# Kernel optimization log

Measured on AMD Instinct MI355X. Metric: run time of the kernel, lower is better.

## Reference

```python
import jax, jax.numpy as jnp
import numpy as np
import math

D = 768       # hidden_size
FF = 3072     # intermediate_size
H = 12        # num heads
L = 3         # decoder_num_hidden_layers
R = 4         # max_role_embeddings
CS = 512      # const_size
B = 256
C = 32
EPS = 1e-5


def _inorm(x):
    # InstanceNorm1d with affine=False on (N, C, L): normalize over last dim
    m = jnp.mean(x, axis=-1, keepdims=True)
    v = jnp.var(x, axis=-1, keepdims=True)
    return (x - m) * jax.lax.rsqrt(v + EPS)


def _mlp(x, w1, b1, w2, b2):
    h = jax.nn.gelu(x @ w1.T + b1, approximate=False)
    return h @ w2.T + b2


def _tree_layer(x, pe, iw, ib, ow, ob, w1, b1, w2, b2):
    # x: (N, 2, D); pe: (N, 2, D)
    qk_in = x + pe
    Wq, Wk, Wv = jnp.split(iw, 3, axis=0)
    bq, bk, bv = jnp.split(ib, 3)
    N = x.shape[0]
    hd = D // H
    q = (qk_in @ Wq.T + bq).reshape(N, 2, H, hd)
    k = (qk_in @ Wk.T + bk).reshape(N, 2, H, hd)
    v = (x @ Wv.T + bv).reshape(N, 2, H, hd)
    scores = jnp.einsum('nqhd,nkhd->nhqk', q, k) / math.sqrt(hd)
    a = jax.nn.softmax(scores, axis=-1)
    o = jnp.einsum('nhqk,nkhd->nqhd', a, v).reshape(N, 2, D)
    o = o @ ow.T + ob
    x = _inorm(x + o)
    f = jax.nn.gelu(x @ w1.T + b1, approximate=False) @ w2.T + b2
    x = _inorm(x + f)
    return x


def setup_inputs() -> dict:
    key = jax.random.key(0)
    ks = jax.random.split(key, 24)
    rn = lambda k, shape, s=0.02: jax.random.normal(k, shape, jnp.float32) * s
    inp = {
        'parent_ij': jax.random.normal(ks[0], (B, D), jnp.float32),
        'child_ikj': jax.random.normal(ks[1], (B, C, 2, D), jnp.float32),
        'parent_scores': jax.random.normal(ks[2], (B, 1), jnp.float32),
        'child_scores': jax.random.normal(ks[3], (B, C, 2), jnp.float32),
        'attn_in_w': rn(ks[4], (L, 3 * D, D)),
        'attn_in_b': rn(ks[5], (L, 3 * D)),
        'attn_out_w': rn(ks[6], (L, D, D)),
        'attn_out_b': rn(ks[7], (L, D)),
        'lin1_w': rn(ks[8], (L, FF, D)),
        'lin1_b': rn(ks[9], (L, FF)),
        'lin2_w': rn(ks[10], (L, D, FF)),
        'lin2_b': rn(ks[11], (L, D)),
        'pos_emb': rn(ks[12], (L, R, D)),
        'parent_w1': rn(ks[13], (D, D)), 'parent_b1': rn(ks[14], (D,)),
        'parent_w2': rn(ks[15], (CS, D)), 'parent_b2': rn(ks[16], (CS,)),
        'left_w1': rn(ks[17], (D, D)), 'left_b1': rn(ks[18], (D,)),
        'left_w2': rn(ks[19], (CS, D)), 'left_b2': rn(ks[20], (CS,)),
        'right_w1': rn(ks[21], (D, D)), 'right_b1': rn(ks[22], (D,)),
        'right_w2': rn(ks[23], (CS, D)), 'right_b2': rn(jax.random.fold_in(key, 99), (CS,)),
    }
    return inp


def reference(parent_ij, child_ikj, parent_scores, child_scores,
              attn_in_w, attn_in_b, attn_out_w, attn_out_b,
              lin1_w, lin1_b, lin2_w, lin2_b, pos_emb,
              parent_w1, parent_b1, parent_w2, parent_b2,
              left_w1, left_b1, left_w2, left_b2,
              right_w1, right_b1, right_w2, right_b2):
    b, c = child_ikj.shape[0], child_ikj.shape[1]
    N = b * c * 2
    # inputs: token0 = parent, token1 = flipped child; row parity 0 -> right child, 1 -> left child
    parent_ext = jnp.broadcast_to(parent_ij[:, None, None, :], (b, c, 2, D))
    child_flip = child_ikj[:, :, ::-1, :]
    x = jnp.stack([parent_ext, child_flip], axis=3).reshape(N, 2, D)

    # scoring heads (parent row is identical for even/odd rows)
    pc = _mlp(parent_ij, parent_w1, parent_b1, parent_w2, parent_b2)          # (b, CS)
    rc = _mlp(child_ikj[:, :, 1, :], right_w1, right_b1, right_w2, right_b2)  # (b, c, CS)
    lc = _mlp(child_ikj[:, :, 0, :], left_w1, left_b1, left_w2, left_b2)      # (b, c, CS)
    scale = 1.0 / math.sqrt(CS)
    left_score = jnp.einsum('bs,bcs->bc', pc, rc) * scale
    right_score = jnp.einsum('bs,bcs->bc', pc, lc) * scale
    outside_scores = jnp.stack([left_score, right_score], axis=2)  # (b, c, 2)

    role_ids = jnp.array([[0, 1], [0, 2]])  # (2, 2) roles for even/odd rows
    for l in range(L):
        pe = jnp.broadcast_to(pos_emb[l][role_ids][None], (b * c, 2, 2, D)).reshape(N, 2, D)
        x = _tree_layer(x, pe, attn_in_w[l], attn_in_b[l], attn_out_w[l], attn_out_b[l],
                        lin1_w[l], lin1_b[l], lin2_w[l], lin2_b[l])

    out_e_ij = _inorm(x.sum(axis=1)).reshape(b, c, 2, D)
    return outside_scores, out_e_ij
```

## Files before the change

kernel.cpp:

```cpp
#include <hip/hip_runtime.h>
#include <cstdint>
#include <cmath>

#define DD      768
#define FFD     3072
#define NH      12
#define HDIM    64
#define LAYERS  3
#define CSZ     512
#define NB      256
#define NC      32
#define NSEQ    (NB * NC * 2)
#define NTOK    (NSEQ * 2)

typedef unsigned short ushort_t;
using short8 = __attribute__((ext_vector_type(8))) short;
using f32x4  = __attribute__((ext_vector_type(4))) float;

static __device__ __forceinline__ float b2f(ushort_t u) {
    union { float f; uint32_t i; } x; x.i = ((uint32_t)u) << 16; return x.f;
}
static __device__ __forceinline__ ushort_t f2b(float f) {
    uint32_t i = __float_as_uint(f);
    uint32_t r = (i + 0x7fffu + ((i >> 16) & 1u)) >> 16;
    return (ushort_t)r;
}
static __device__ __forceinline__ float gelu_f(float x) {
    return 0.5f * x * (1.0f + erff(x * 0.70710678118654752f));
}
static __device__ __forceinline__ float wave_sum64(float v) {
#pragma unroll
    for (int off = 32; off > 0; off >>= 1) v += __shfl_xor(v, off, 64);
    return v;
}
static __device__ __forceinline__ void async_cp16(const void* g, void* l) {
    __builtin_amdgcn_global_load_lds((const __attribute__((address_space(1))) void*)g,
                                     (__attribute__((address_space(3))) void*)l, 16, 0, 0);
}
static __device__ __forceinline__ void wg_barrier() {
    asm volatile("" ::: "memory");
    __builtin_amdgcn_s_barrier();
    asm volatile("" ::: "memory");
}
#define WAITVM(N) asm volatile("s_waitcnt vmcnt(" #N ")" ::: "memory")
#define LDSFENCE() asm volatile("s_waitcnt lgkmcnt(0)" ::: "memory")

__global__ __launch_bounds__(256) void cvt_bf16(const float* __restrict__ s,
                                                ushort_t* __restrict__ d, int n) {
    const int i = (blockIdx.x * 256 + threadIdx.x) * 4;
    if (i < n) {
        const float4 v = *(const float4*)(s + i);
        ushort4 o;
        o.x = f2b(v.x); o.y = f2b(v.y); o.z = f2b(v.z); o.w = f2b(v.w);
        *(ushort4*)(d + i) = o;
    }
}

__global__ __launch_bounds__(192) void build_x(const float* __restrict__ parent,
                                               const float* __restrict__ child,
                                               ushort_t* __restrict__ X) {
    const int r = blockIdx.x;
    const int t = threadIdx.x;
    const int n = r >> 1, q = r & 1;
    const int i = n >> 6;
    const int k = (n >> 1) & 31;
    const int j = n & 1;
    const float* src = (q == 0) ? (parent + (size_t)i * DD)
                                : (child + ((size_t)((i * 32 + k) * 2 + (1 - j))) * DD);
    const float4 v = ((const float4*)src)[t];
    ushort4 o;
    o.x = f2b(v.x); o.y = f2b(v.y); o.z = f2b(v.z); o.w = f2b(v.w);
    ((ushort4*)(X + (size_t)r * DD))[t] = o;
}

__global__ __launch_bounds__(256) void gemm_bf16(const ushort_t* __restrict__ A, int lda,
                                                 const ushort_t* __restrict__ W,
                                                 const float* __restrict__ bias,
                                                 ushort_t* __restrict__ C, int ldc,
                                                 int K, int NT, int GM, int GN,
                                                 int dogelu) {
    __shared__ __align__(16) short smem[16384];
    short* As = smem;
    short* Bs = smem + 8192;

    const int st = blockIdx.x / (GM * GN);
    const int stn = NT / GN;
    const int srow = st / stn, scol = st - srow * stn;
    const int r = blockIdx.x - st * (GM * GN);
    const int mt = srow * GM + r / GN;
    const int nt = scol * GN + (r - (r / GN) * GN);
    const int m0 = mt * 128;
    const int n0 = nt * 128;

    const int tid = threadIdx.x;
    const int r0s = tid >> 2, c0s = (tid & 3) * 8;
    const ushort_t* Ag0 = A + (size_t)(m0 + r0s) * lda + c0s;
    const ushort_t* Ag1 = A + (size_t)(m0 + 64 + r0s) * lda + c0s;
    const ushort_t* Wg0 = W + (size_t)(n0 + r0s) * K + c0s;
    const ushort_t* Wg1 = W + (size_t)(n0 + 64 + r0s) * K + c0s;

    const int wid = tid >> 6, lane = tid & 63;
    const int wm = (wid >> 1) * 64, wn = (wid & 1) * 64;
    const int lm = lane & 15;
    const int ko = (lane >> 4) * 8;

    f32x4 acc[4][4];
#pragma unroll
    for (int i = 0; i < 4; ++i)
#pragma unroll
        for (int j = 0; j < 4; ++j) acc[i][j] = {0.f, 0.f, 0.f, 0.f};

    {
        async_cp16(Ag0, As + tid * 8);
        async_cp16(Ag1, As + 2048 + tid * 8);
        async_cp16(Wg0, Bs + tid * 8);
        async_cp16(Wg1, Bs + 2048 + tid * 8);
    }

    for (int k0 = 0; k0 < K; k0 += 32) {
        const int b = (k0 >> 5) & 1;
        const int boff = b * 4096;
        __syncthreads();
        if (k0 + 32 < K) {
            const int o = (boff ^ 4096);
            const int k = k0 + 32;
            async_cp16(Ag0 + k, As + o + tid * 8);
            async_cp16(Ag1 + k, As + o + 2048 + tid * 8);
            async_cp16(Wg0 + k, Bs + o + tid * 8);
            async_cp16(Wg1 + k, Bs + o + 2048 + tid * 8);
        }
        short8 af[4], bfr[4];
#pragma unroll
        for (int i = 0; i < 4; ++i)
            af[i] = *(const short8*)(As + boff + (wm + i * 16 + lm) * 32 + ko);
#pragma unroll
        for (int j = 0; j < 4; ++j)
            bfr[j] = *(const short8*)(Bs + boff + (wn + j * 16 + lm) * 32 + ko);
#pragma unroll
        for (int i = 0; i < 4; ++i)
#pragma unroll
            for (int j = 0; j < 4; ++j)
                acc[i][j] = __builtin_amdgcn_mfma_f32_16x16x32_bf16(af[i], bfr[j], acc[i][j], 0, 0, 0);
    }

    float* T = (float*)smem;
    float* Tw = T + wid * 1088;
    const int r4 = lane >> 4;
    const int rrow = lane >> 2;
    const int rc0 = (lane & 3) * 16;
    const int gcolb = n0 + wn;

    float4 bb[4];
    if (bias) {
#pragma unroll
        for (int t = 0; t < 4; ++t) bb[t] = *(const float4*)(bias + gcolb + rc0 + t * 4);
    } else {
#pragma unroll
        for (int t = 0; t < 4; ++t) bb[t] = make_float4(0.f, 0.f, 0.f, 0.f);
    }

#pragma unroll
    for (int i = 0; i < 4; ++i) {
        __syncthreads();
#pragma unroll
        for (int j = 0; j < 4; ++j)
#pragma unroll
            for (int rr = 0; rr < 4; ++rr)
                Tw[(r4 * 4 + rr) * 68 + j * 16 + lm] = acc[i][j][rr];
        __syncthreads();
        float o[16];
#pragma unroll
        for (int t = 0; t < 4; ++t)
            *(f32x4*)&o[t * 4] = *(const f32x4*)(Tw + rrow * 68 + rc0 + t * 4);
#pragma unroll
        for (int t = 0; t < 4; ++t) {
            o[t * 4 + 0] += ((const float*)&bb[t])[0];
            o[t * 4 + 1] += ((const float*)&bb[t])[1];
            o[t * 4 + 2] += ((const float*)&bb[t])[2];
            o[t * 4 + 3] += ((const float*)&bb[t])[3];
        }
        if (dogelu) {
#pragma unroll
            for (int t = 0; t < 16; ++t) o[t] = gelu_f(o[t]);
        }
        uint32_t pk[8];
#pragma unroll
        for (int t = 0; t < 8; ++t)
            pk[t] = (uint32_t)f2b(o[2 * t]) | ((uint32_t)f2b(o[2 * t + 1]) << 16);
        ushort_t* dst = C + (size_t)(m0 + wm + i * 16 + rrow) * ldc + gcolb + rc0;
        *(uint4*)dst = make_uint4(pk[0], pk[1], pk[2], pk[3]);
        *(uint4*)(dst + 8) = make_uint4(pk[4], pk[5], pk[6], pk[7]);
    }
}

__global__ __launch_bounds__(512, 2) void gemm256(const ushort_t* __restrict__ A, int lda,
                                                  const ushort_t* __restrict__ W,
                                                  const float* __restrict__ bias,
                                                  ushort_t* __restrict__ C, int ldc,
                                                  int K, int NT, int GM, int GN,
                                                  int dogelu) {
    __shared__ __align__(16) short smem[65536];
    const int tid = threadIdx.x;

    const int nwg = gridDim.x;
    const int bid = blockIdx.x;
    const int qx = nwg >> 3, rx = nwg & 7;
    const int xcd = bid & 7, pos = bid >> 3;
    const int wgid = (xcd < rx ? xcd * (qx + 1) : rx * (qx + 1) + (xcd - rx) * qx) + pos;
    const int stb = GM * GN;
    const int st = wgid / stb;
    const int stn = NT / GN;
    const int srow = st / stn, scol = st - srow * stn;
    const int r = wgid - st * stb;
    const int mt = srow * GM + r / GN;
    const int nt = scol * GN + (r - (r / GN) * GN);
    const int m0 = mt * 256, n0 = nt * 256;

    const int srow_t = tid >> 2;
    const int scol_t = ((tid & 3) ^ ((tid >> 3) & 3)) << 3;
    const ushort_t* Ag = A + (size_t)(m0 + srow_t) * lda + scol_t;
    const ushort_t* Bg = W + (size_t)(n0 + srow_t) * K + scol_t;
    short* ldsA = smem + tid * 8;
    short* ldsB = smem + 8192 + tid * 8;
    const size_t ldaH = (size_t)128 * lda;
    const size_t ldbH = (size_t)128 * K;

    auto stage2A = [&](int kt_) {
        const int b_ = (kt_ & 3) * 16384;
        const int k_ = kt_ * 32;
        async_cp16(Ag + k_,        ldsA + b_);
        async_cp16(Ag + ldaH + k_, ldsA + b_ + 4096);
    };
    auto stage2B = [&](int kt_) {
        const int b_ = (kt_ & 3) * 16384;
        const int k_ = kt_ * 32;
        async_cp16(Bg + k_,        ldsB + b_);
        async_cp16(Bg + ldbH + k_, ldsB + b_ + 4096);
    };

    const int wid = tid >> 6, lane = tid & 63;
    const int wr = wid >> 2, wc = wid & 3;
    const int lm = lane & 15;
    const int swz = (((lane >> 4) ^ ((lane >> 1) & 3)) << 3);
    const short* rdA = smem + (wr * 128 + lm) * 32 + swz;
    const short* rdB = smem + 8192 + (wc * 64 + lm) * 32 + swz;

    f32x4 acc[8][4];
#pragma unroll
    for (int i = 0; i < 8; ++i)
#pragma unroll
        for (int j = 0; j < 4; ++j) acc[i][j] = {0.f, 0.f, 0.f, 0.f};

    const int NKT = K >> 5;
    stage2A(0); stage2B(0); stage2A(1); stage2B(1); stage2A(2); stage2B(2);
    WAITVM(8);
    wg_barrier();

    for (int kt = 0; kt < NKT; ++kt) {
        const int boff = (kt & 3) * 16384;
        short8 af[4], bfr[4], ag[4];
#pragma unroll
        for (int j = 0; j < 4; ++j) bfr[j] = *(const short8*)(rdB + boff + j * 512);
#pragma unroll
        for (int i = 0; i < 4; ++i) af[i] = *(const short8*)(rdA + boff + i * 512);
        if (kt + 3 < NKT) stage2A(kt + 3);
        wg_barrier();
        LDSFENCE();
        __builtin_amdgcn_s_setprio(1);
#pragma unroll
        for (int i = 0; i < 4; ++i)
#pragma unroll
            for (int j = 0; j < 4; ++j)
                acc[i][j] = __builtin_amdgcn_mfma_f32_16x16x32_bf16(af[i], bfr[j], acc[i][j], 0, 0, 0);
        __builtin_amdgcn_s_setprio(0);
        wg_barrier();
#pragma unroll
        for (int i = 0; i < 4; ++i) ag[i] = *(const short8*)(rdA + boff + (4 + i) * 512);
        if (kt + 3 < NKT) stage2B(kt + 3);
        if (kt + 3 < NKT)      { WAITVM(8); }
        else if (kt + 2 < NKT) { WAITVM(4); }
        else                   { WAITVM(0); }
        wg_barrier();
        LDSFENCE();
        __builtin_amdgcn_s_setprio(1);
#pragma unroll
        for (int i = 0; i < 4; ++i)
#pragma unroll
            for (int j = 0; j < 4; ++j)
                acc[4 + i][j] = __builtin_amdgcn_mfma_f32_16x16x32_bf16(ag[i], bfr[j], acc[4 + i][j], 0, 0, 0);
        __builtin_amdgcn_s_setprio(0);
        wg_barrier();
    }

    float* T = (float*)smem;
    float* Tw = T + wid * 1088;
    const int r4 = lane >> 4;
    const int rrow = lane >> 2;
    const int rc0 = (lane & 3) * 16;
    const int gcolb = n0 + wc * 64;

    float4 bb[4];
#pragma unroll
    for (int t = 0; t < 4; ++t) bb[t] = *(const float4*)(bias + gcolb + rc0 + t * 4);

#pragma unroll
    for (int mi = 0; mi < 8; ++mi) {
#pragma unroll
        for (int j = 0; j < 4; ++j)
#pragma unroll
            for (int rr = 0; rr < 4; ++rr)
                Tw[(r4 * 4 + rr) * 68 + j * 16 + lm] = acc[mi][j][rr];
        LDSFENCE();
        float o[16];
#pragma unroll
        for (int t = 0; t < 4; ++t)
            *(f32x4*)&o[t * 4] = *(const f32x4*)(Tw + rrow * 68 + rc0 + t * 4);
#pragma unroll
        for (int t = 0; t < 4; ++t) {
            o[t * 4 + 0] += ((const float*)&bb[t])[0];
            o[t * 4 + 1] += ((const float*)&bb[t])[1];
            o[t * 4 + 2] += ((const float*)&bb[t])[2];
            o[t * 4 + 3] += ((const float*)&bb[t])[3];
        }
        if (dogelu) {
#pragma unroll
            for (int t = 0; t < 16; ++t) o[t] = gelu_f(o[t]);
        }
        uint32_t pk[8];
#pragma unroll
        for (int t = 0; t < 8; ++t)
            pk[t] = (uint32_t)f2b(o[2 * t]) | ((uint32_t)f2b(o[2 * t + 1]) << 16);
        ushort_t* dst = C + (size_t)(m0 + wr * 128 + mi * 16 + rrow) * ldc + gcolb + rc0;
        *(uint4*)dst = make_uint4(pk[0], pk[1], pk[2], pk[3]);
        *(uint4*)(dst + 8) = make_uint4(pk[4], pk[5], pk[6], pk[7]);
        LDSFENCE();
    }
}

__global__ __launch_bounds__(256) void pe_proj(const float* __restrict__ pel,
                                               const float* __restrict__ aiwl,
                                               float* __restrict__ PEQ,
                                               float* __restrict__ PEK) {
    const int wid = threadIdx.x >> 6, lane = threadIdx.x & 63;
    const int task = blockIdx.x * 4 + wid;
    const int which = task >= 3 * DD;
    const int idx = task - which * 3 * DD;
    const int r = idx / DD, o = idx - r * DD;
    const float* pe = pel + (size_t)r * DD;
    const float* w = aiwl + (size_t)(which ? DD + o : o) * DD;
    float s = 0.f;
#pragma unroll
    for (int e = 0; e < 12; ++e) s += pe[e * 64 + lane] * w[e * 64 + lane];
    s = wave_sum64(s);
    if (lane == 0) (which ? PEK : PEQ)[r * DD + o] = s;
}

__global__ __launch_bounds__(256) void attn_kernel(const ushort_t* __restrict__ QKV,
                                                   const float* __restrict__ peq,
                                                   const float* __restrict__ pek,
                                                   ushort_t* __restrict__ O,
                                                   int seq0) {
    const int wid = threadIdx.x >> 6;
    const int lane = threadIdx.x & 63;
    const int task = blockIdx.x * 4 + wid;
    const int ns = task / NH;
    const int h = task - ns * NH;
    const int j = (seq0 + ns) & 1;
    const ushort_t* base = QKV + (size_t)(2 * ns) * (3 * DD);
    const int c = h * HDIM + lane;
    const int role1 = (1 + j) * DD;

    const float q0 = b2f(base[c]) + peq[c];
    const float k0 = b2f(base[DD + c]) + pek[c];
    const float v0 = b2f(base[2 * DD + c]);
    const ushort_t* base1 = base + 3 * DD;
    const float q1 = b2f(base1[c]) + peq[role1 + c];
    const float k1 = b2f(base1[DD + c]) + pek[role1 + c];
    const float v1 = b2f(base1[2 * DD + c]);

    float p00 = q0 * k0, p01 = q0 * k1, p10 = q1 * k0, p11 = q1 * k1;
#pragma unroll
    for (int off = 32; off > 0; off >>= 1) {
        p00 += __shfl_xor(p00, off, 64);
        p01 += __shfl_xor(p01, off, 64);
        p10 += __shfl_xor(p10, off, 64);
        p11 += __shfl_xor(p11, off, 64);
    }
    const float sc = 0.125f;
    const float s00 = p00 * sc, s01 = p01 * sc, s10 = p10 * sc, s11 = p11 * sc;

    const float m0 = fmaxf(s00, s01);
    const float e00 = __expf(s00 - m0), e01 = __expf(s01 - m0);
    const float a00 = e00 / (e00 + e01);
    const float o0 = a00 * v0 + (1.0f - a00) * v1;

    const float m1 = fmaxf(s10, s11);
    const float e10 = __expf(s10 - m1), e11 = __expf(s11 - m1);
    const float a10 = e10 / (e10 + e11);
    const float o1 = a10 * v0 + (1.0f - a10) * v1;

    O[(size_t)(2 * ns) * DD + c] = f2b(o0);
    O[(size_t)(2 * ns + 1) * DD + c] = f2b(o1);
}

__global__ __launch_bounds__(256) void add_inorm(ushort_t* __restrict__ x,
                                                 const ushort_t* __restrict__ d) {
    const int wid = threadIdx.x >> 6, lane = threadIdx.x & 63;
    const int r = blockIdx.x * 4 + wid;
    ushort_t* xr = x + (size_t)r * DD;
    const ushort_t* dr = d + (size_t)r * DD;
    float v[12];
    float s = 0.f, ss = 0.f;
#pragma unroll
    for (int e = 0; e < 3; ++e) {
        const ushort4 xa = ((const ushort4*)xr)[e * 64 + lane];
        const ushort4 da = ((const ushort4*)dr)[e * 64 + lane];
        const float a0 = b2f(xa.x) + b2f(da.x);
        const float a1 = b2f(xa.y) + b2f(da.y);
        const float a2 = b2f(xa.z) + b2f(da.z);
        const float a3 = b2f(xa.w) + b2f(da.w);
        v[e * 4 + 0] = a0; v[e * 4 + 1] = a1; v[e * 4 + 2] = a2; v[e * 4 + 3] = a3;
        s += a0 + a1 + a2 + a3;
        ss += a0 * a0 + a1 * a1 + a2 * a2 + a3 * a3;
    }
    s = wave_sum64(s); ss = wave_sum64(ss);
    const float mean = s * (1.0f / DD);
    const float var = ss * (1.0f / DD) - mean * mean;
    const float rs = rsqrtf(var + 1e-5f);
#pragma unroll
    for (int e = 0; e < 3; ++e) {
        ushort4 o;
        o.x = f2b((v[e * 4 + 0] - mean) * rs);
        o.y = f2b((v[e * 4 + 1] - mean) * rs);
        o.z = f2b((v[e * 4 + 2] - mean) * rs);
        o.w = f2b((v[e * 4 + 3] - mean) * rs);
        ((ushort4*)xr)[e * 64 + lane] = o;
    }
}

__global__ __launch_bounds__(256) void final_inorm(const ushort_t* __restrict__ x,
                                                   float* __restrict__ out) {
    const int wid = threadIdx.x >> 6, lane = threadIdx.x & 63;
    const int n = blockIdx.x * 4 + wid;
    const ushort_t* r0 = x + (size_t)(2 * n) * DD;
    const ushort_t* r1 = r0 + DD;
    float v[12];
    float s = 0.f, ss = 0.f;
#pragma unroll
    for (int e = 0; e < 3; ++e) {
        const ushort4 xa = ((const ushort4*)r0)[e * 64 + lane];
        const ushort4 xb = ((const ushort4*)r1)[e * 64 + lane];
        const float a0 = b2f(xa.x) + b2f(xb.x);
        const float a1 = b2f(xa.y) + b2f(xb.y);
        const float a2 = b2f(xa.z) + b2f(xb.z);
        const float a3 = b2f(xa.w) + b2f(xb.w);
        v[e * 4 + 0] = a0; v[e * 4 + 1] = a1; v[e * 4 + 2] = a2; v[e * 4 + 3] = a3;
        s += a0 + a1 + a2 + a3;
        ss += a0 * a0 + a1 * a1 + a2 * a2 + a3 * a3;
    }
    s = wave_sum64(s); ss = wave_sum64(ss);
    const float mean = s * (1.0f / DD);
    const float var = ss * (1.0f / DD) - mean * mean;
    const float rs = rsqrtf(var + 1e-5f);
    float* orow = out + (size_t)n * DD;
#pragma unroll
    for (int e = 0; e < 3; ++e) {
        float4 o;
        o.x = (v[e * 4 + 0] - mean) * rs;
        o.y = (v[e * 4 + 1] - mean) * rs;
        o.z = (v[e * 4 + 2] - mean) * rs;
        o.w = (v[e * 4 + 3] - mean) * rs;
        ((float4*)orow)[e * 64 + lane] = o;
    }
}

__global__ __launch_bounds__(256) void score_dot(const ushort_t* __restrict__ pc,
                                                 const ushort_t* __restrict__ cc,
                                                 float* __restrict__ out, int which) {
    const int wid = threadIdx.x >> 6;
    const int lane = threadIdx.x & 63;
    const int row = blockIdx.x * 4 + wid;
    const int b = row >> 5;
    const ushort_t* p = pc + (size_t)b * CSZ;
    const ushort_t* c = cc + (size_t)row * CSZ;
    float s = 0.f;
#pragma unroll
    for (int e = 0; e < 8; ++e) s += b2f(p[e * 64 + lane]) * b2f(c[e * 64 + lane]);
    s = wave_sum64(s);
    if (lane == 0) out[row * 2 + which] = s * 0.04419417382415922f;
}

extern "C" void kernel_launch(void* const* d_in, const int* in_sizes, int n_in,
                              void* d_out, int out_size, void* d_ws, size_t ws_size,
                              hipStream_t stream) {
    const float* parent = (const float*)d_in[0];
    const float* child  = (const float*)d_in[1];
    const float* aiw = (const float*)d_in[4];
    const float* aib = (const float*)d_in[5];
    const float* aow = (const float*)d_in[6];
    const float* aob = (const float*)d_in[7];
    const float* l1w = (const float*)d_in[8];
    const float* l1b = (const float*)d_in[9];
    const float* l2w = (const float*)d_in[10];
    const float* l2b = (const float*)d_in[11];
    const float* pemb = (const float*)d_in[12];
    const float* pw1 = (const float*)d_in[13];
    const float* pb1 = (const float*)d_in[14];
    const float* pw2 = (const float*)d_in[15];
    const float* pb2 = (const float*)d_in[16];
    const float* lw1 = (const float*)d_in[17];
    const float* lb1 = (const float*)d_in[18];
    const float* lw2 = (const float*)d_in[19];
    const float* lb2 = (const float*)d_in[20];
    const float* rw1 = (const float*)d_in[21];
    const float* rb1 = (const float*)d_in[22];
    const float* rw2 = (const float*)d_in[23];
    const float* rb2 = (const float*)d_in[24];
    float* out = (float*)d_out;
    (void)in_sizes; (void)n_in; (void)out_size;

    int CH = 8192;
    {
        const size_t fixedB = 100ull * 1024 * 1024;
        if (ws_size >= fixedB + (size_t)32768 * 4608 * 2) CH = 32768;
        else if (ws_size >= fixedB + (size_t)16384 * 4608 * 2) CH = 16384;
    }
    const int NCH = NTOK / CH;

    ushort_t* W0 = (ushort_t*)d_ws;
    size_t off = 0;
    auto take = [&](size_t elems) { ushort_t* p = W0 + off; off += (elems + 127) & ~(size_t)127; return p; };
    ushort_t* aiw_b = take((size_t)LAYERS * 3 * DD * DD);
    ushort_t* aow_b = take((size_t)LAYERS * DD * DD);
    ushort_t* l1w_b = take((size_t)LAYERS * FFD * DD);
    ushort_t* l2w_b = take((size_t)LAYERS * DD * FFD);
    ushort_t* pw1_b = take((size_t)DD * DD);
    ushort_t* pw2_b = take((size_t)CSZ * DD);
    ushort_t* lw1_b = take((size_t)DD * DD);
    ushort_t* lw2_b = take((size_t)CSZ * DD);
    ushort_t* rw1_b = take((size_t)DD * DD);
    ushort_t* rw2_b = take((size_t)CSZ * DD);
    ushort_t* Pb    = take((size_t)NB * DD);
    ushort_t* Xb    = take((size_t)NTOK * DD);
    ushort_t* S1b   = take((size_t)CH * FFD);
    ushort_t* S2b   = take((size_t)CH * DD);
    ushort_t* S3b   = take((size_t)CH * DD);
    ushort_t* P1b   = take((size_t)NB * DD);
    ushort_t* P2b   = take((size_t)NB * CSZ);
    float* PEQ = (float*)(W0 + off); off += 2 * 3 * DD;
    float* PEK = PEQ + 3 * DD;

    auto cvt = [&](const float* s, ushort_t* d, size_t n) {
        cvt_bf16<<<(int)((n + 1023) / 1024), 256, 0, stream>>>(s, d, (int)n);
    };
    auto gemm = [&](const ushort_t* A, int lda, const ushort_t* Wt, const float* bias,
                    ushort_t* C, int ldc, int M, int N, int K, int dg) {
        if (M % 256 == 0 && N % 256 == 0 && M >= 8192 && N >= 768 && K >= 96 && K % 32 == 0) {
            const int MT = M / 256, NT = N / 256;
            const int GM = (MT % 8 == 0) ? 8 : ((MT % 4 == 0) ? 4 : MT);
            int GN = 8;
            while (NT % GN) --GN;
            gemm256<<<MT * NT, 512, 0, stream>>>(A, lda, Wt, bias, C, ldc, K, NT, GM, GN, dg);
        } else {
            const int MT = M / 128, NT = N / 128;
            const int GM = (MT % 8 == 0) ? 8 : MT;
            int GN = 8;
            while (NT % GN) --GN;
            gemm_bf16<<<MT * NT, 256, 0, stream>>>(A, lda, Wt, bias, C, ldc, K, NT, GM, GN, dg);
        }
    };

    cvt(aiw, aiw_b, (size_t)LAYERS * 3 * DD * DD);
    cvt(aow, aow_b, (size_t)LAYERS * DD * DD);
    cvt(l1w, l1w_b, (size_t)LAYERS * FFD * DD);
    cvt(l2w, l2w_b, (size_t)LAYERS * DD * FFD);
    cvt(pw1, pw1_b, (size_t)DD * DD);
    cvt(pw2, pw2_b, (size_t)CSZ * DD);
    cvt(lw1, lw1_b, (size_t)DD * DD);
    cvt(lw2, lw2_b, (size_t)CSZ * DD);
    cvt(rw1, rw1_b, (size_t)DD * DD);
    cvt(rw2, rw2_b, (size_t)CSZ * DD);
    cvt(parent, Pb, (size_t)NB * DD);
    cvt(child, S1b, (size_t)NB * NC * 2 * DD);

    build_x<<<NTOK, 192, 0, stream>>>(parent, child, Xb);

    gemm(Pb, DD, pw1_b, pb1, P1b, DD, NB, DD, DD, 1);
    gemm(P1b, DD, pw2_b, pb2, P2b, CSZ, NB, CSZ, DD, 0);
    gemm(S1b, 2 * DD, lw1_b, lb1, S2b, DD, NB * NC, DD, DD, 1);
    gemm(S2b, DD, lw2_b, lb2, S3b, CSZ, NB * NC, CSZ, DD, 0);
    score_dot<<<NB * NC / 4, 256, 0, stream>>>(P2b, S3b, out, 1);
    gemm(S1b + DD, 2 * DD, rw1_b, rb1, S2b, DD, NB * NC, DD, DD, 1);
    gemm(S2b, DD, rw2_b, rb2, S3b, CSZ, NB * NC, CSZ, DD, 0);
    score_dot<<<NB * NC / 4, 256, 0, stream>>>(P2b, S3b, out, 0);

    for (int l = 0; l < LAYERS; ++l) {
        const ushort_t* Wl  = aiw_b + (size_t)l * 3 * DD * DD;
        const float* bl  = aib + (size_t)l * 3 * DD;
        const ushort_t* owl = aow_b + (size_t)l * DD * DD;
        const float* obl = aob + (size_t)l * DD;
        const ushort_t* w1l = l1w_b + (size_t)l * FFD * DD;
        const float* b1l = l1b + (size_t)l * FFD;
        const ushort_t* w2l = l2w_b + (size_t)l * DD * FFD;
        const float* b2l = l2b + (size_t)l * DD;

        pe_proj<<<2 * 3 * DD / 4, 256, 0, stream>>>(pemb + (size_t)l * 4 * DD,
                                                    aiw + (size_t)l * 3 * DD * DD, PEQ, PEK);

        for (int c = 0; c < NCH; ++c) {
            ushort_t* Xc = Xb + (size_t)c * CH * DD;
            gemm(Xc, DD, Wl, bl, S1b, 3 * DD, CH, 3 * DD, DD, 0);
            attn_kernel<<<(CH / 2) * NH / 4, 256, 0, stream>>>(S1b, PEQ, PEK, S2b, c * (CH / 2));
            gemm(S2b, DD, owl, obl, S3b, DD, CH, DD, DD, 0);
            add_inorm<<<CH / 4, 256, 0, stream>>>(Xc, S3b);
            gemm(Xc, DD, w1l, b1l, S1b, FFD, CH, FFD, DD, 1);
            gemm(S1b, FFD, w2l, b2l, S3b, DD, CH, DD, FFD, 0);
            add_inorm<<<CH / 4, 256, 0, stream>>>(Xc, S3b);
        }
    }

    final_inorm<<<NSEQ / 4, 256, 0, stream>>>(Xb, out + NSEQ);
}
```

Measured before the change: 2.587 ms.

## Software-pipeline LDS fragment loads across k-tiles in 256x256 GEMM

New measurement: 2.549 ms. No clear change (-1.5%).

```diff
diff --git a/kernel.cpp b/kernel.cpp
--- a/kernel.cpp
+++ b/kernel.cpp
@@ -43,7 +43,9 @@
     asm volatile("" ::: "memory");
 }
 #define WAITVM(N) asm volatile("s_waitcnt vmcnt(" #N ")" ::: "memory")
+#define LGKM(N)   asm volatile("s_waitcnt lgkmcnt(" #N ")" ::: "memory")
 #define LDSFENCE() asm volatile("s_waitcnt lgkmcnt(0)" ::: "memory")
+#define SCHEDBAR() __builtin_amdgcn_sched_barrier(0)
 
 __global__ __launch_bounds__(256) void cvt_bf16(const float* __restrict__ s,
                                                 ushort_t* __restrict__ d, int n) {
@@ -251,45 +253,62 @@
 #pragma unroll
         for (int j = 0; j < 4; ++j) acc[i][j] = {0.f, 0.f, 0.f, 0.f};
 
+    short8 af[4], ag[4], bE[4], bO[4];
     const int NKT = K >> 5;
+
     stage2A(0); stage2B(0); stage2A(1); stage2B(1); stage2A(2); stage2B(2);
     WAITVM(8);
     wg_barrier();
-
-    for (int kt = 0; kt < NKT; ++kt) {
+#pragma unroll
+    for (int j = 0; j < 4; ++j) bE[j] = *(const short8*)(rdB + j * 512);
+#pragma unroll
+    for (int i = 0; i < 4; ++i) af[i] = *(const short8*)(rdA + i * 512);
+
+    auto tile_body = [&](int kt, short8 (&Bc)[4], short8 (&Bn)[4]) {
         const int boff = (kt & 3) * 16384;
-        short8 af[4], bfr[4], ag[4];
-#pragma unroll
-        for (int j = 0; j < 4; ++j) bfr[j] = *(const short8*)(rdB + boff + j * 512);
-#pragma unroll
-        for (int i = 0; i < 4; ++i) af[i] = *(const short8*)(rdA + boff + i * 512);
+        wg_barrier();
+#pragma unroll
+        for (int i = 0; i < 4; ++i) ag[i] = *(const short8*)(rdA + boff + (4 + i) * 512);
         if (kt + 3 < NKT) stage2A(kt + 3);
-        wg_barrier();
-        LDSFENCE();
+        LGKM(4);
+        SCHEDBAR();
         __builtin_amdgcn_s_setprio(1);
 #pragma unroll
         for (int i = 0; i < 4; ++i)
 #pragma unroll
             for (int j = 0; j < 4; ++j)
-                acc[i][j] = __builtin_amdgcn_mfma_f32_16x16x32_bf16(af[i], bfr[j], acc[i][j], 0, 0, 0);
+                acc[i][j] = __builtin_amdgcn_mfma_f32_16x16x32_bf16(af[i], Bc[j], acc[i][j], 0, 0, 0);
         __builtin_amdgcn_s_setprio(0);
-        wg_barrier();
-#pragma unroll
-        for (int i = 0; i < 4; ++i) ag[i] = *(const short8*)(rdA + boff + (4 + i) * 512);
+        SCHEDBAR();
         if (kt + 3 < NKT) stage2B(kt + 3);
         if (kt + 3 < NKT)      { WAITVM(8); }
         else if (kt + 2 < NKT) { WAITVM(4); }
         else                   { WAITVM(0); }
         wg_barrier();
-        LDSFENCE();
+        if (kt + 1 < NKT) {
+            const int nboff = ((kt + 1) & 3) * 16384;
+#pragma unroll
+            for (int j = 0; j < 4; ++j) Bn[j] = *(const short8*)(rdB + nboff + j * 512);
+#pragma unroll
+            for (int i = 0; i < 4; ++i) af[i] = *(const short8*)(rdA + nboff + i * 512);
+            LGKM(8);
+        } else {
+            LGKM(0);
+        }
+        SCHEDBAR();
         __builtin_amdgcn_s_setprio(1);
 #pragma unroll
         for (int i = 0; i < 4; ++i)
 #pragma unroll
             for (int j = 0; j < 4; ++j)
-                acc[4 + i][j] = __builtin_amdgcn_mfma_f32_16x16x32_bf16(ag[i], bfr[j], acc[4 + i][j], 0, 0, 0);
+                acc[4 + i][j] = __builtin_amdgcn_mfma_f32_16x16x32_bf16(ag[i], Bc[j], acc[4 + i][j], 0, 0, 0);
         __builtin_amdgcn_s_setprio(0);
-        wg_barrier();
+        SCHEDBAR();
+    };
+
+    for (int kt = 0; kt < NKT; kt += 2) {
+        tile_body(kt, bE, bO);
+        tile_body(kt + 1, bO, bE);
     }
 
     float* T = (float*)smem;
@@ -555,7 +574,7 @@
     };
     auto gemm = [&](const ushort_t* A, int lda, const ushort_t* Wt, const float* bias,
                     ushort_t* C, int ldc, int M, int N, int K, int dg) {
-        if (M % 256 == 0 && N % 256 == 0 && M >= 8192 && N >= 768 && K >= 96 && K % 32 == 0) {
+        if (M % 256 == 0 && N % 256 == 0 && M >= 8192 && N >= 768 && K >= 384 && K % 64 == 0) {
             const int MT = M / 256, NT = N / 256;
             const int GM = (MT % 8 == 0) ? 8 : ((MT % 4 == 0) ? 4 : MT);
             int GN = 8;
```
